# Optimization experiments

Measured on AMD Instinct MI355X. Metric: run time of the kernel, lower is better.

Reference implementation:

```python
import jax, jax.numpy as jnp
import numpy as np

B, N, D, P, V = 8, 256, 300, 128, 50001  # batch, seq len, emb dim, proj dim, vocab(+unk)


def setup_inputs() -> dict:
    key = jax.random.key(0)
    ks = jax.random.split(key, 10)
    s = 1.0 / np.sqrt(D)
    sp = 1.0 / np.sqrt(P)
    emb = jax.random.normal(ks[0], (V, D), jnp.float32)
    emb = emb.at[-1].set(0.0)  # unk row zeroed, matches add_unk
    return {
        "sentence": jax.random.randint(ks[1], (B, N), 0, V),
        "emb": emb,
        "Wl": jax.random.uniform(ks[2], (P, D), jnp.float32, -s, s),
        "bl": jnp.zeros((P,), jnp.float32),
        "Wr": jax.random.uniform(ks[3], (P, D), jnp.float32, -s, s),
        "Wo": jax.random.uniform(ks[4], (1, P), jnp.float32, -sp, sp),
        "bo": jnp.zeros((1,), jnp.float32),
        "Ws1": jax.random.uniform(ks[5], (P, D), jnp.float32, -s, s),
        "bs1": jnp.zeros((P,), jnp.float32),
        "Ws2": jax.random.uniform(ks[6], (1, P), jnp.float32, -sp, sp),
        "bs2": jnp.zeros((1,), jnp.float32),
        "We1": jax.random.uniform(ks[7], (P, D), jnp.float32, -s, s),
        "be1": jnp.zeros((P,), jnp.float32),
        "We2": jax.random.uniform(ks[8], (1, P), jnp.float32, -sp, sp),
        "be2": jnp.zeros((1,), jnp.float32),
    }


def reference(sentence, emb, Wl, bl, Wr, Wo, bo, Ws1, bs1, Ws2, bs2, We1, be1, We2, be2):
    x = emb[sentence]                                   # [B,N,D] embedding lookup
    start = jax.nn.relu(x @ Ws1.T + bs1) @ Ws2.T + bs2  # [B,N,1]
    end = jax.nn.relu(x @ We1.T + be1) @ We2.T + be2    # [B,N,1]
    left = x @ Wl.T + bl                                # [B,N,P]
    right = x @ Wr.T                                    # [B,N,P]
    # proj[b,i,j,p] = left[b,j,p] + right[b,i,p]  (unsqueeze(1) + unsqueeze(2))
    proj = left[:, None, :, :] + right[:, :, None, :]   # [B,N,N,P]
    bigram = jax.nn.relu(proj) @ Wo.T + bo              # [B,N,N,1]
    return (bigram, start, end)
```

## Files before the change

### kernel.cpp

```cpp
#include <hip/hip_runtime.h>

#define NB 8
#define NN 256
#define DD 300
#define PP 128
#define NC 512
#define OFF_S (NB * NN * NN)
#define OFF_E (NB * NN * NN + NB * NN)

typedef unsigned short u16;
typedef unsigned int   u32;

__device__ __forceinline__ float bf2f(u16 u) {
    union { u32 i; float f; } v;
    v.i = ((u32)u) << 16;
    return v.f;
}
__device__ __forceinline__ u16 f2bf(float f) {
    union { float f; u32 i; } v;
    v.f = f;
    u32 lsb = (v.i >> 16) & 1u;
    v.i += 0x7fffu + lsb;
    return (u16)(v.i >> 16);
}

template<bool BF>
__device__ __forceinline__ float4 ld4(const void* base, int idx) {
    if (BF) {
        ushort4 e = *(const ushort4*)((const u16*)base + idx);
        return make_float4(bf2f(e.x), bf2f(e.y), bf2f(e.z), bf2f(e.w));
    } else {
        return *(const float4*)((const float*)base + idx);
    }
}
template<bool BF>
__device__ __forceinline__ float ld1(const void* base, int idx) {
    return BF ? bf2f(((const u16*)base)[idx]) : ((const float*)base)[idx];
}
template<bool BF>
__device__ __forceinline__ void st1(void* base, int idx, float v) {
    if (BF) ((u16*)base)[idx] = f2bf(v);
    else    ((float*)base)[idx] = v;
}
template<bool BF>
__device__ __forceinline__ void st4(void* base, int idx, float4 v) {
    if (BF) {
        ushort4 o = make_ushort4(f2bf(v.x), f2bf(v.y), f2bf(v.z), f2bf(v.w));
        *(ushort4*)((u16*)base + idx) = o;
    } else {
        *(float4*)((float*)base + idx) = v;
    }
}
__device__ __forceinline__ float4 rfma4(float4 l, float r, float w, float4 a) {
    a.x = fmaf(fmaxf(l.x + r, 0.f), w, a.x);
    a.y = fmaf(fmaxf(l.y + r, 0.f), w, a.y);
    a.z = fmaf(fmaxf(l.z + r, 0.f), w, a.z);
    a.w = fmaf(fmaxf(l.w + r, 0.f), w, a.w);
    return a;
}

extern "C" __global__ void detect_kernel(const u32* __restrict__ embU,
                                         int* __restrict__ flag) {
    int lane = threadIdx.x;
    int cnt = 0;
    for (int i = lane; i < 256; i += 64) {
        u32 w = embU[i];
        union { u32 u; float f; } v;
        v.u = (w & 0xFFFFu) << 16;
        float a = fabsf(v.f);
        if (a == 0.f || (a >= 0.00390625f && a <= 256.f)) cnt++;
    }
    #pragma unroll
    for (int off = 32; off; off >>= 1) cnt += __shfl_down(cnt, off, 64);
    if (lane == 0) *flag = (cnt >= 128) ? 1 : 0;
}

template<bool BF>
__device__ __forceinline__ void prep_body(
    const void* __restrict__ Wl, const void* __restrict__ Wr,
    const void* __restrict__ Ws1, const void* __restrict__ We1,
    float* __restrict__ WTf, float (*tile)[301])
{
    const int tid = threadIdx.x;
    const int c0  = blockIdx.x * 32;

    for (int e = tid; e < 32 * 75; e += 256) {
        int r = e / 75;
        int q = e - r * 75;
        int c = c0 + r;
        const void* src = (c < 128) ? Wl : (c < 256) ? Wr
                        : (c < 384) ? Ws1 : We1;
        float4 f = ld4<BF>(src, (c & 127) * DD + 4 * q);
        tile[r][4 * q + 0] = f.x;
        tile[r][4 * q + 1] = f.y;
        tile[r][4 * q + 2] = f.z;
        tile[r][4 * q + 3] = f.w;
    }
    __syncthreads();
    for (int e = tid; e < 300 * 32; e += 256) {
        int k = e >> 5;
        int c = e & 31;
        WTf[(size_t)k * NC + c0 + c] = tile[c][k];
    }
}

extern "C" __global__ void __launch_bounds__(256)
prep_kernel(const void* __restrict__ Wl, const void* __restrict__ Wr,
            const void* __restrict__ Ws1, const void* __restrict__ We1,
            float* __restrict__ WTf, const int* __restrict__ flag)
{
    __shared__ float tile[32][301];
    if (*flag) prep_body<true >(Wl, Wr, Ws1, We1, WTf, tile);
    else       prep_body<false>(Wl, Wr, Ws1, We1, WTf, tile);
}

template<bool BF>
__device__ __forceinline__ void tok_body(
    const int* __restrict__ sent, const void* __restrict__ emb,
    const float* __restrict__ WTf,
    const void* __restrict__ bl,
    const void* __restrict__ bs1, const void* __restrict__ Ws2,
    const void* __restrict__ bs2,
    const void* __restrict__ be1, const void* __restrict__ We2,
    const void* __restrict__ be2,
    float* __restrict__ leftT, float* __restrict__ rightW,
    void* __restrict__ out, float (*sxT)[4], int* sids)
{
    const int tid = threadIdx.x;
    const int t0  = blockIdx.x * 4;

    if (tid < 4) sids[tid] = sent[t0 + tid];
    __syncthreads();

    for (int e = tid; e < DD * 4; e += 256) {
        int k = e >> 2, t = e & 3;
        sxT[k][t] = ld1<BF>(emb, sids[t] * DD + k);
    }
    __syncthreads();

    float a0[4], a1[4];
    #pragma unroll
    for (int t = 0; t < 4; ++t) { a0[t] = 0.f; a1[t] = 0.f; }

    const float* wp = WTf + 2 * tid;
    #pragma unroll 4
    for (int k = 0; k < DD; ++k) {
        float2 w  = *(const float2*)(wp + (size_t)k * NC);
        float4 xa = *(const float4*)&sxT[k][0];
        a0[0] = fmaf(xa.x, w.x, a0[0]); a1[0] = fmaf(xa.x, w.y, a1[0]);
        a0[1] = fmaf(xa.y, w.x, a0[1]); a1[1] = fmaf(xa.y, w.y, a1[1]);
        a0[2] = fmaf(xa.z, w.x, a0[2]); a1[2] = fmaf(xa.z, w.y, a1[2]);
        a0[3] = fmaf(xa.w, w.x, a0[3]); a1[3] = fmaf(xa.w, w.y, a1[3]);
    }

    const int wv = tid >> 6;
    const int l  = tid & 63;
    const int p0 = 2 * l, p1 = p0 + 1;

    if (wv == 0) {
        float b0 = ld1<BF>(bl, p0), b1 = ld1<BF>(bl, p1);
        #pragma unroll
        for (int t = 0; t < 4; ++t) {
            int tg = t0 + t, bb = tg >> 8, jj = tg & 255;
            leftT[((size_t)bb * PP + p0) * NN + jj] = a0[t] + b0;
            leftT[((size_t)bb * PP + p1) * NN + jj] = a1[t] + b1;
        }
    } else if (wv == 1) {
        #pragma unroll
        for (int t = 0; t < 4; ++t) {
            rightW[(size_t)(t0 + t) * PP + p0] = a0[t];
            rightW[(size_t)(t0 + t) * PP + p1] = a1[t];
        }
    } else {
        const void* h1 = (wv == 2) ? bs1 : be1;
        const void* h2 = (wv == 2) ? Ws2 : We2;
        const void* h3 = (wv == 2) ? bs2 : be2;
        float b0 = ld1<BF>(h1, p0), b1 = ld1<BF>(h1, p1);
        float w0 = ld1<BF>(h2, p0), w1 = ld1<BF>(h2, p1);
        float v[4];
        #pragma unroll
        for (int t = 0; t < 4; ++t)
            v[t] = fmaxf(a0[t] + b0, 0.f) * w0 + fmaxf(a1[t] + b1, 0.f) * w1;
        #pragma unroll
        for (int off = 32; off; off >>= 1) {
            #pragma unroll
            for (int t = 0; t < 4; ++t) v[t] += __shfl_down(v[t], off, 64);
        }
        if (l == 0) {
            float b2 = ld1<BF>(h3, 0);
            int base = (wv == 2) ? OFF_S : OFF_E;
            #pragma unroll
            for (int t = 0; t < 4; ++t)
                st1<BF>(out, base + t0 + t, v[t] + b2);
        }
    }
}

extern "C" __global__ void __launch_bounds__(256)
tok_kernel(const int* __restrict__ sent, const void* __restrict__ emb,
           const float* __restrict__ WTf,
           const void* __restrict__ bl,
           const void* __restrict__ bs1, const void* __restrict__ Ws2,
           const void* __restrict__ bs2,
           const void* __restrict__ be1, const void* __restrict__ We2,
           const void* __restrict__ be2,
           float* __restrict__ leftT, float* __restrict__ rightW,
           void* __restrict__ out, const int* __restrict__ flag)
{
    __shared__ __align__(16) float sxT[DD][4];
    __shared__ int sids[4];
    if (*flag) {
        tok_body<true >(sent, emb, WTf, bl, bs1, Ws2, bs2, be1, We2, be2,
                        leftT, rightW, out, sxT, sids);
    } else {
        tok_body<false>(sent, emb, WTf, bl, bs1, Ws2, bs2, be1, We2, be2,
                        leftT, rightW, out, sxT, sids);
    }
}

template<bool BF>
__device__ __forceinline__ void big_body(
    const float* __restrict__ leftT, const float* __restrict__ rightW,
    const void* __restrict__ Wo, const void* __restrict__ bo,
    void* __restrict__ outB,
    float (*sR)[128], float* sWo, float4 (*red4)[64][4])
{
    const int tid = threadIdx.x;
    const int b   = blockIdx.x >> 6;
    const int i0  = (blockIdx.x & 63) << 2;

    if (tid < 128) sWo[tid] = ld1<BF>(Wo, tid);
    for (int c = tid; c < 512; c += 256) {
        int i = c >> 7, pp = c & 127;
        sR[i][pp] = rightW[((size_t)(b * NN + i0 + i)) * PP + pp];
    }
    __syncthreads();

    const int w    = tid >> 6;
    const int lane = tid & 63;
    const int j4   = lane << 2;
    const float* lp = leftT + (size_t)b * PP * NN + j4;

    float4 A0 = {0.f, 0.f, 0.f, 0.f}, A1 = A0, A2 = A0, A3 = A0;
    const int pbase = w * 32;
    #pragma unroll
    for (int g = 0; g < 8; ++g) {
        const int p = pbase + g * 4;
        float4 wo = *(const float4*)&sWo[p];
        float4 r0 = *(const float4*)&sR[0][p];
        float4 r1 = *(const float4*)&sR[1][p];
        float4 r2 = *(const float4*)&sR[2][p];
        float4 r3 = *(const float4*)&sR[3][p];
        const float* lpp = lp + (size_t)p * NN;
        float4 l0 = *(const float4*)(lpp);
        float4 l1 = *(const float4*)(lpp + NN);
        float4 l2 = *(const float4*)(lpp + 2 * NN);
        float4 l3 = *(const float4*)(lpp + 3 * NN);
        A0 = rfma4(l0, r0.x, wo.x, A0);
        A1 = rfma4(l0, r1.x, wo.x, A1);
        A2 = rfma4(l0, r2.x, wo.x, A2);
        A3 = rfma4(l0, r3.x, wo.x, A3);
        A0 = rfma4(l1, r0.y, wo.y, A0);
        A1 = rfma4(l1, r1.y, wo.y, A1);
        A2 = rfma4(l1, r2.y, wo.y, A2);
        A3 = rfma4(l1, r3.y, wo.y, A3);
        A0 = rfma4(l2, r0.z, wo.z, A0);
        A1 = rfma4(l2, r1.z, wo.z, A1);
        A2 = rfma4(l2, r2.z, wo.z, A2);
        A3 = rfma4(l2, r3.z, wo.z, A3);
        A0 = rfma4(l3, r0.w, wo.w, A0);
        A1 = rfma4(l3, r1.w, wo.w, A1);
        A2 = rfma4(l3, r2.w, wo.w, A2);
        A3 = rfma4(l3, r3.w, wo.w, A3);
    }

    red4[w][lane][0] = A0;
    red4[w][lane][1] = A1;
    red4[w][lane][2] = A2;
    red4[w][lane][3] = A3;
    __syncthreads();

    if (tid < 64) {
        float bov = ld1<BF>(bo, 0);
        #pragma unroll
        for (int i = 0; i < 4; ++i) {
            float4 s0 = red4[0][tid][i];
            float4 s1 = red4[1][tid][i];
            float4 s2 = red4[2][tid][i];
            float4 s3 = red4[3][tid][i];
            float4 s;
            s.x = s0.x + s1.x + s2.x + s3.x + bov;
            s.y = s0.y + s1.y + s2.y + s3.y + bov;
            s.z = s0.z + s1.z + s2.z + s3.z + bov;
            s.w = s0.w + s1.w + s2.w + s3.w + bov;
            st4<BF>(outB, (int)(((size_t)(b * NN + i0 + i)) * NN) + tid * 4, s);
        }
    }
}

extern "C" __global__ void __launch_bounds__(256)
big_kernel(const float* __restrict__ leftT, const float* __restrict__ rightW,
           const void* __restrict__ Wo, const void* __restrict__ bo,
           void* __restrict__ outB, const int* __restrict__ flag)
{
    __shared__ float sR[4][128];
    __shared__ float sWo[128];
    __shared__ float4 red4[4][64][4];
    if (*flag) big_body<true >(leftT, rightW, Wo, bo, outB, sR, sWo, red4);
    else       big_body<false>(leftT, rightW, Wo, bo, outB, sR, sWo, red4);
}

extern "C" void kernel_launch(void* const* d_in, const int* in_sizes, int n_in,
                              void* d_out, int out_size, void* d_ws, size_t ws_size,
                              hipStream_t stream) {
    const int*  sent = (const int*)d_in[0];
    const void* emb  = d_in[1];
    const void* Wl   = d_in[2];
    const void* bl   = d_in[3];
    const void* Wr   = d_in[4];
    const void* Wo   = d_in[5];
    const void* bo   = d_in[6];
    const void* Ws1  = d_in[7];
    const void* bs1  = d_in[8];
    const void* Ws2  = d_in[9];
    const void* bs2  = d_in[10];
    const void* We1  = d_in[11];
    const void* be1  = d_in[12];
    const void* We2  = d_in[13];
    const void* be2  = d_in[14];

    int*   flag   = (int*)d_ws;
    float* leftT  = (float*)((char*)d_ws + 1024);
    float* rightW = leftT + (size_t)NB * PP * NN;
    float* WTf    = rightW + (size_t)NB * NN * PP;

    hipLaunchKernelGGL(detect_kernel, dim3(1), dim3(64), 0, stream,
                       (const u32*)emb, flag);
    hipLaunchKernelGGL(prep_kernel, dim3(16), dim3(256), 0, stream,
                       Wl, Wr, Ws1, We1, WTf, flag);
    hipLaunchKernelGGL(tok_kernel, dim3(512), dim3(256), 0, stream,
                       sent, emb, WTf, bl, bs1, Ws2, bs2, be1, We2, be2,
                       leftT, rightW, d_out, flag);
    hipLaunchKernelGGL(big_kernel, dim3(512), dim3(256), 0, stream,
                       leftT, rightW, Wo, bo, d_out, flag);
}
```

Measured before the change: 158.8 us.

## Pre-gather embeddings in prep kernel and widen token projection register tiles

The embedding gather moves into the prep kernel, which now has 32 extra blocks that write the gathered rows as fp32 into a workspace buffer. The token kernel then reads those rows directly instead of staging them in shared memory. Each thread of the token kernel now computes a 4-column by 4-token tile, and a block covers 8 tokens, halving the block count and raising weight reuse per load. The cost is an extra global write and read of the gathered embeddings, plus scalar, uncoalesced x loads that rely on the cache.

```diff
diff --git a/kernel.cpp b/kernel.cpp
--- a/kernel.cpp
+++ b/kernel.cpp
@@ -79,126 +79,156 @@
 __device__ __forceinline__ void prep_body(
     const void* __restrict__ Wl, const void* __restrict__ Wr,
     const void* __restrict__ Ws1, const void* __restrict__ We1,
-    float* __restrict__ WTf, float (*tile)[301])
+    const int* __restrict__ sent, const void* __restrict__ emb,
+    float* __restrict__ WTf, float* __restrict__ xf, float (*tile)[301])
 {
     const int tid = threadIdx.x;
-    const int c0  = blockIdx.x * 32;
-
-    for (int e = tid; e < 32 * 75; e += 256) {
-        int r = e / 75;
-        int q = e - r * 75;
-        int c = c0 + r;
-        const void* src = (c < 128) ? Wl : (c < 256) ? Wr
-                        : (c < 384) ? Ws1 : We1;
-        float4 f = ld4<BF>(src, (c & 127) * DD + 4 * q);
-        tile[r][4 * q + 0] = f.x;
-        tile[r][4 * q + 1] = f.y;
-        tile[r][4 * q + 2] = f.z;
-        tile[r][4 * q + 3] = f.w;
-    }
-    __syncthreads();
-    for (int e = tid; e < 300 * 32; e += 256) {
-        int k = e >> 5;
-        int c = e & 31;
-        WTf[(size_t)k * NC + c0 + c] = tile[c][k];
+
+    if (blockIdx.x < 16) {
+        const int c0 = blockIdx.x * 32;
+        for (int e = tid; e < 32 * 75; e += 256) {
+            int r = e / 75;
+            int q = e - r * 75;
+            int c = c0 + r;
+            const void* src = (c < 128) ? Wl : (c < 256) ? Wr
+                            : (c < 384) ? Ws1 : We1;
+            float4 f = ld4<BF>(src, (c & 127) * DD + 4 * q);
+            tile[r][4 * q + 0] = f.x;
+            tile[r][4 * q + 1] = f.y;
+            tile[r][4 * q + 2] = f.z;
+            tile[r][4 * q + 3] = f.w;
+        }
+        __syncthreads();
+        for (int e = tid; e < 300 * 32; e += 256) {
+            int k = e >> 5;
+            int c = e & 31;
+            WTf[(size_t)k * NC + c0 + c] = tile[c][k];
+        }
+    } else {
+        const int t0g = (blockIdx.x - 16) * 64;
+        for (int e = tid; e < 64 * DD; e += 256) {
+            int t = e / DD;
+            int k = e - t * DD;
+            int idx = sent[t0g + t];
+            xf[(size_t)(t0g + t) * DD + k] = ld1<BF>(emb, idx * DD + k);
+        }
     }
 }
 
 extern "C" __global__ void __launch_bounds__(256)
 prep_kernel(const void* __restrict__ Wl, const void* __restrict__ Wr,
             const void* __restrict__ Ws1, const void* __restrict__ We1,
-            float* __restrict__ WTf, const int* __restrict__ flag)
+            const int* __restrict__ sent, const void* __restrict__ emb,
+            float* __restrict__ WTf, float* __restrict__ xf,
+            const int* __restrict__ flag)
 {
     __shared__ float tile[32][301];
-    if (*flag) prep_body<true >(Wl, Wr, Ws1, We1, WTf, tile);
-    else       prep_body<false>(Wl, Wr, Ws1, We1, WTf, tile);
+    if (*flag) prep_body<true >(Wl, Wr, Ws1, We1, sent, emb, WTf, xf, tile);
+    else       prep_body<false>(Wl, Wr, Ws1, We1, sent, emb, WTf, xf, tile);
 }
 
 template<bool BF>
 __device__ __forceinline__ void tok_body(
-    const int* __restrict__ sent, const void* __restrict__ emb,
-    const float* __restrict__ WTf,
+    const float* __restrict__ WTf, const float* __restrict__ xf,
     const void* __restrict__ bl,
     const void* __restrict__ bs1, const void* __restrict__ Ws2,
     const void* __restrict__ bs2,
     const void* __restrict__ be1, const void* __restrict__ We2,
     const void* __restrict__ be2,
     float* __restrict__ leftT, float* __restrict__ rightW,
-    void* __restrict__ out, float (*sxT)[4], int* sids)
-{
-    const int tid = threadIdx.x;
-    const int t0  = blockIdx.x * 4;
-
-    if (tid < 4) sids[tid] = sent[t0 + tid];
-    __syncthreads();
-
-    for (int e = tid; e < DD * 4; e += 256) {
-        int k = e >> 2, t = e & 3;
-        sxT[k][t] = ld1<BF>(emb, sids[t] * DD + k);
-    }
-    __syncthreads();
-
-    float a0[4], a1[4];
-    #pragma unroll
-    for (int t = 0; t < 4; ++t) { a0[t] = 0.f; a1[t] = 0.f; }
-
-    const float* wp = WTf + 2 * tid;
+    void* __restrict__ out)
+{
+    const int tid   = threadIdx.x;
+    const int t0    = blockIdx.x * 8;
+    const int half  = tid >> 7;
+    const int l127  = tid & 127;
+    const int col4  = l127 * 4;
+    const int tbase = t0 + 4 * half;
+
+    const float* x0 = xf + (size_t)(tbase + 0) * DD;
+    const float* x1 = xf + (size_t)(tbase + 1) * DD;
+    const float* x2 = xf + (size_t)(tbase + 2) * DD;
+    const float* x3 = xf + (size_t)(tbase + 3) * DD;
+    const float* wrow = WTf + col4;
+
+    float a0[4] = {0,0,0,0}, a1[4] = {0,0,0,0};
+    float a2[4] = {0,0,0,0}, a3[4] = {0,0,0,0};
+
     #pragma unroll 4
     for (int k = 0; k < DD; ++k) {
-        float2 w  = *(const float2*)(wp + (size_t)k * NC);
-        float4 xa = *(const float4*)&sxT[k][0];
-        a0[0] = fmaf(xa.x, w.x, a0[0]); a1[0] = fmaf(xa.x, w.y, a1[0]);
-        a0[1] = fmaf(xa.y, w.x, a0[1]); a1[1] = fmaf(xa.y, w.y, a1[1]);
-        a0[2] = fmaf(xa.z, w.x, a0[2]); a1[2] = fmaf(xa.z, w.y, a1[2]);
-        a0[3] = fmaf(xa.w, w.x, a0[3]); a1[3] = fmaf(xa.w, w.y, a1[3]);
-    }
-
-    const int wv = tid >> 6;
-    const int l  = tid & 63;
-    const int p0 = 2 * l, p1 = p0 + 1;
-
-    if (wv == 0) {
-        float b0 = ld1<BF>(bl, p0), b1 = ld1<BF>(bl, p1);
-        #pragma unroll
-        for (int t = 0; t < 4; ++t) {
-            int tg = t0 + t, bb = tg >> 8, jj = tg & 255;
-            leftT[((size_t)bb * PP + p0) * NN + jj] = a0[t] + b0;
-            leftT[((size_t)bb * PP + p1) * NN + jj] = a1[t] + b1;
-        }
-    } else if (wv == 1) {
-        #pragma unroll
-        for (int t = 0; t < 4; ++t) {
-            rightW[(size_t)(t0 + t) * PP + p0] = a0[t];
-            rightW[(size_t)(t0 + t) * PP + p1] = a1[t];
-        }
-    } else {
-        const void* h1 = (wv == 2) ? bs1 : be1;
-        const void* h2 = (wv == 2) ? Ws2 : We2;
-        const void* h3 = (wv == 2) ? bs2 : be2;
-        float b0 = ld1<BF>(h1, p0), b1 = ld1<BF>(h1, p1);
-        float w0 = ld1<BF>(h2, p0), w1 = ld1<BF>(h2, p1);
+        float4 w = *(const float4*)(wrow + (size_t)k * NC);
+        float s0 = x0[k], s1 = x1[k], s2 = x2[k], s3 = x3[k];
+        a0[0] = fmaf(w.x, s0, a0[0]); a0[1] = fmaf(w.y, s0, a0[1]);
+        a0[2] = fmaf(w.z, s0, a0[2]); a0[3] = fmaf(w.w, s0, a0[3]);
+        a1[0] = fmaf(w.x, s1, a1[0]); a1[1] = fmaf(w.y, s1, a1[1]);
+        a1[2] = fmaf(w.z, s1, a1[2]); a1[3] = fmaf(w.w, s1, a1[3]);
+        a2[0] = fmaf(w.x, s2, a2[0]); a2[1] = fmaf(w.y, s2, a2[1]);
+        a2[2] = fmaf(w.z, s2, a2[2]); a2[3] = fmaf(w.w, s2, a2[3]);
+        a3[0] = fmaf(w.x, s3, a3[0]); a3[1] = fmaf(w.y, s3, a3[1]);
+        a3[2] = fmaf(w.z, s3, a3[2]); a3[3] = fmaf(w.w, s3, a3[3]);
+    }
+
+    const int m = l127 >> 5;
+    const int p = col4 & 127;
+
+    if (m == 0) {
+        float b[4];
+        #pragma unroll
+        for (int r = 0; r < 4; ++r) b[r] = ld1<BF>(bl, p + r);
+        const int bb = tbase >> 8;
+        #pragma unroll
+        for (int tt = 0; tt < 4; ++tt) {
+            const int jj = (tbase + tt) & 255;
+            float* acc = (tt == 0) ? a0 : (tt == 1) ? a1 : (tt == 2) ? a2 : a3;
+            #pragma unroll
+            for (int r = 0; r < 4; ++r)
+                leftT[((size_t)bb * PP + p + r) * NN + jj] = acc[r] + b[r];
+        }
+    } else if (m == 1) {
+        #pragma unroll
+        for (int tt = 0; tt < 4; ++tt) {
+            float* acc = (tt == 0) ? a0 : (tt == 1) ? a1 : (tt == 2) ? a2 : a3;
+            *(float4*)(rightW + (size_t)(tbase + tt) * PP + p) =
+                make_float4(acc[0], acc[1], acc[2], acc[3]);
+        }
+    } else {
+        const void* h1 = (m == 2) ? bs1 : be1;
+        const void* h2 = (m == 2) ? Ws2 : We2;
+        const void* h3 = (m == 2) ? bs2 : be2;
+        float b1[4], w2[4];
+        #pragma unroll
+        for (int r = 0; r < 4; ++r) {
+            b1[r] = ld1<BF>(h1, p + r);
+            w2[r] = ld1<BF>(h2, p + r);
+        }
         float v[4];
         #pragma unroll
-        for (int t = 0; t < 4; ++t)
-            v[t] = fmaxf(a0[t] + b0, 0.f) * w0 + fmaxf(a1[t] + b1, 0.f) * w1;
-        #pragma unroll
-        for (int off = 32; off; off >>= 1) {
+        for (int tt = 0; tt < 4; ++tt) {
+            float* acc = (tt == 0) ? a0 : (tt == 1) ? a1 : (tt == 2) ? a2 : a3;
+            float s = 0.f;
             #pragma unroll
-            for (int t = 0; t < 4; ++t) v[t] += __shfl_down(v[t], off, 64);
-        }
-        if (l == 0) {
+            for (int r = 0; r < 4; ++r)
+                s += fmaxf(acc[r] + b1[r], 0.f) * w2[r];
+            v[tt] = s;
+        }
+        #pragma unroll
+        for (int off = 16; off; off >>= 1) {
+            #pragma unroll
+            for (int tt = 0; tt < 4; ++tt)
+                v[tt] += __shfl_down(v[tt], off, 32);
+        }
+        if ((l127 & 31) == 0) {
             float b2 = ld1<BF>(h3, 0);
-            int base = (wv == 2) ? OFF_S : OFF_E;
+            int base = (m == 2) ? OFF_S : OFF_E;
             #pragma unroll
-            for (int t = 0; t < 4; ++t)
-                st1<BF>(out, base + t0 + t, v[t] + b2);
+            for (int tt = 0; tt < 4; ++tt)
+                st1<BF>(out, base + tbase + tt, v[tt] + b2);
         }
     }
 }
 
 extern "C" __global__ void __launch_bounds__(256)
-tok_kernel(const int* __restrict__ sent, const void* __restrict__ emb,
-           const float* __restrict__ WTf,
+tok_kernel(const float* __restrict__ WTf, const float* __restrict__ xf,
            const void* __restrict__ bl,
            const void* __restrict__ bs1, const void* __restrict__ Ws2,
            const void* __restrict__ bs2,
@@ -207,14 +237,12 @@
            float* __restrict__ leftT, float* __restrict__ rightW,
            void* __restrict__ out, const int* __restrict__ flag)
 {
-    __shared__ __align__(16) float sxT[DD][4];
-    __shared__ int sids[4];
     if (*flag) {
-        tok_body<true >(sent, emb, WTf, bl, bs1, Ws2, bs2, be1, We2, be2,
-                        leftT, rightW, out, sxT, sids);
-    } else {
-        tok_body<false>(sent, emb, WTf, bl, bs1, Ws2, bs2, be1, We2, be2,
-                        leftT, rightW, out, sxT, sids);
+        tok_body<true >(WTf, xf, bl, bs1, Ws2, bs2, be1, We2, be2,
+                        leftT, rightW, out);
+    } else {
+        tok_body<false>(WTf, xf, bl, bs1, Ws2, bs2, be1, We2, be2,
+                        leftT, rightW, out);
     }
 }
 
@@ -333,13 +361,14 @@
     float* leftT  = (float*)((char*)d_ws + 1024);
     float* rightW = leftT + (size_t)NB * PP * NN;
     float* WTf    = rightW + (size_t)NB * NN * PP;
+    float* xf     = WTf + (size_t)DD * NC;
 
     hipLaunchKernelGGL(detect_kernel, dim3(1), dim3(64), 0, stream,
                        (const u32*)emb, flag);
-    hipLaunchKernelGGL(prep_kernel, dim3(16), dim3(256), 0, stream,
-                       Wl, Wr, Ws1, We1, WTf, flag);
-    hipLaunchKernelGGL(tok_kernel, dim3(512), dim3(256), 0, stream,
-                       sent, emb, WTf, bl, bs1, Ws2, bs2, be1, We2, be2,
+    hipLaunchKernelGGL(prep_kernel, dim3(48), dim3(256), 0, stream,
+                       Wl, Wr, Ws1, We1, sent, emb, WTf, xf, flag);
+    hipLaunchKernelGGL(tok_kernel, dim3(256), dim3(256), 0, stream,
+                       WTf, xf, bl, bs1, Ws2, bs2, be1, We2, be2,
                        leftT, rightW, d_out, flag);
     hipLaunchKernelGGL(big_kernel, dim3(512), dim3(256), 0, stream,
                        leftT, rightW, Wo, bo, d_out, flag);
```

Result: slower. 182.3 us (+14.8%).
